# Kernel optimization log

Hardware: AMD Instinct MI355X
Metric: run time of the kernel (lower is better)

Reference implementation:

```python
import jax, jax.numpy as jnp
import numpy as np
from jax.scipy.special import logsumexp

B, T = 8192, 1024  # batch, timesteps; n_states = 2 (BKT: not-know / know)


def setup_inputs() -> dict:
    key = jax.random.key(0)
    k1, k2, k3 = jax.random.split(key, 3)
    corr = jax.random.randint(k1, (B, T), 0, 2)  # binary observations
    dynamics_logits = jax.random.normal(k2, (B, 3), dtype=jnp.float32)  # (pL, pF, pI0) logits
    obs_logits = jax.random.normal(k3, (B, T, 2), dtype=jnp.float32)  # (pG, pS) logits per step
    return {"corr": corr, "dynamics_logits": dynamics_logits, "obs_logits": obs_logits}


def _get_logits(dynamics_logits, obs_logits):
    # trans_logits[b] = [[0, d1],[d0, 0]]  (target, source)
    z = jnp.zeros_like(dynamics_logits[:, 0])
    trans_logits = jnp.stack([z, dynamics_logits[:, 1], dynamics_logits[:, 0], z], axis=1).reshape(-1, 2, 2)
    # obs_full[b,t] = [[0, o0],[o1, 0]]  (state, output)
    zo = jnp.zeros_like(obs_logits[:, :, 0])
    obs_full = jnp.stack([zo, obs_logits[:, :, 0], obs_logits[:, :, 1], zo], axis=2)
    obs_full = obs_full.reshape(obs_logits.shape[0], -1, 2, 2)
    # init_logits[b] = [0, d2]
    init_logits = jnp.stack([z, dynamics_logits[:, 2]], axis=1)
    return trans_logits, obs_full, init_logits


def _bkt(corr, dynamics_logits, obs_logits):
    trans_logits, obs_full, init_logits = _get_logits(dynamics_logits, obs_logits)
    log_obs = jax.nn.log_softmax(obs_full, axis=3)   # (B,T,2,2)
    log_t = jax.nn.log_softmax(trans_logits, axis=1)  # (B,2,2) softmax over target state
    log_alpha0 = jax.nn.log_softmax(init_logits, axis=1)  # (B,2)
    lo_t = jnp.moveaxis(log_obs, 1, 0)  # (T,B,2,2)
    y_t = corr.T                        # (T,B)

    def fwd_step(log_alpha, inp):
        lo, y = inp  # lo: (B,2,2), y: (B,)
        # predictive p(y_t | y_1:t-1)
        log_py_pred = logsumexp(lo + log_alpha[:, :, None], axis=1)  # (B,2)
        log_py_pred = log_py_pred - logsumexp(log_py_pred, axis=1, keepdims=True)
        # emission of observed symbol per state
        log_py = jnp.take_along_axis(lo, y[:, None, None], axis=2)[:, :, 0]  # (B,2)
        state_post = log_py + log_alpha  # P(h_t, y_1:t)
        new_alpha = logsumexp(log_py[:, None, :] + log_alpha[:, None, :] + log_t, axis=2)
        return new_alpha, (log_py_pred, state_post)

    _, (preds, posts) = jax.lax.scan(fwd_step, log_alpha0, (lo_t, y_t))
    output_logprobs = jnp.moveaxis(preds, 0, 1)     # (B,T,2)
    state_posteriors = jnp.moveaxis(posts, 0, 1)    # (B,T,2)

    def bwd_step(log_beta, inp):
        lo, y = inp
        log_py = jnp.take_along_axis(lo, y[:, None, None], axis=2)[:, :, 0]  # (B,2)
        new_beta = logsumexp(log_py[:, :, None] + log_beta[:, :, None] + log_t, axis=1)
        return new_beta, log_beta

    beta0 = jnp.zeros_like(log_alpha0)
    _, betas = jax.lax.scan(bwd_step, beta0, (lo_t, y_t), reverse=True)
    backward_logprobs = jnp.moveaxis(betas, 0, 1)  # (B,T,2), time-aligned

    smoothed = state_posteriors + backward_logprobs
    smoothed = smoothed - logsumexp(smoothed, axis=2, keepdims=True)
    # stack the three BxTx2 outputs -> (3,B,T,2)
    return jnp.stack([output_logprobs, state_posteriors, smoothed], axis=0)


def reference(corr, dynamics_logits, obs_logits):
    return _bkt(corr, dynamics_logits, obs_logits)
```

## Files before the change

### kernel.cpp

```cpp
#include <hip/hip_runtime.h>


#define BB 8192
#define TT 1024
#define KC 16
#define NC 64
#define GG 4
#define NTHREADS (GG * NC)
#define NEGI (-1.0e30f)
#define LOG2E 1.4426950408889634f
#define LN2   0.6931471805599453f

typedef float floatx4 __attribute__((ext_vector_type(4)));

__device__ __forceinline__ float fexp2(float x) {
    return __builtin_amdgcn_exp2f(x);
}
__device__ __forceinline__ float flog2(float x) {
    return __builtin_amdgcn_logf(x);
}
__device__ __forceinline__ float softplus2(float x) {
    return fmaxf(x, 0.0f) + flog2(1.0f + fexp2(-fabsf(x)));
}
__device__ __forceinline__ float lse2_2(float a, float b) {
    float m = fmaxf(a, b);
    return m + flog2(1.0f + fexp2(-fabsf(a - b)));
}

__global__ __launch_bounds__(NTHREADS, 4) void bkt_kernel(
        const int* __restrict__ corr,
        const float* __restrict__ dyn,
        const float* __restrict__ obs,
        float* __restrict__ out) {
    __shared__ floatx4 st[GG][NC + 2][8];

    const int tid = threadIdx.x;
    const int g = tid >> 6;
    const int c = tid & (NC - 1);
    const int b = blockIdx.x * GG + g;

    const float d0 = dyn[b * 3 + 0] * LOG2E;
    const float d1 = dyn[b * 3 + 1] * LOG2E;
    const float d2 = dyn[b * 3 + 2] * LOG2E;
    const float sd0 = softplus2(d0), sd1 = softplus2(d1);
    const float lt00 = -sd0, lt10 = d0 - sd0, lt01 = d1 - sd1, lt11 = -sd1;

    const long long cb = (long long)b * TT + c * KC;
    const float2* obs2 = (const float2*)obs;
    const long long S4 = (long long)BB * 512;
    floatx4* o0 = (floatx4*)out;
    floatx4* o1 = o0 + S4;
    floatx4* o2 = o1 + S4;

    float ox[16], oy[16];
    unsigned ybits = 0;
    float F00, F01, F10, F11;
    {
        const float4* op = (const float4*)(obs2 + cb);
        const int4* yp = (const int4*)(corr + cb);
        #pragma unroll
        for (int j = 0; j < 8; ++j) {
            float4 o4 = op[j];
            ox[2 * j]     = o4.x * LOG2E; oy[2 * j]     = o4.y * LOG2E;
            ox[2 * j + 1] = o4.z * LOG2E; oy[2 * j + 1] = o4.w * LOG2E;
        }
        #pragma unroll
        for (int j = 0; j < 4; ++j) {
            int4 y4 = yp[j];
            ybits |= (unsigned)(y4.x & 1) << (4 * j + 0);
            ybits |= (unsigned)(y4.y & 1) << (4 * j + 1);
            ybits |= (unsigned)(y4.z & 1) << (4 * j + 2);
            ybits |= (unsigned)(y4.w & 1) << (4 * j + 3);
        }
        #pragma unroll
        for (int q = 0; q < 16; ++q) {
            float sp0 = softplus2(ox[q]), sp1 = softplus2(oy[q]);
            int y = (ybits >> q) & 1;
            float py0 = y ? (ox[q] - sp0) : (-sp0);
            float py1 = y ? (-sp1) : (oy[q] - sp1);
            float N00 = py0 + lt00, N01 = py1 + lt01;
            float N10 = py0 + lt10, N11 = py1 + lt11;
            if (q == 0) {
                F00 = N00; F01 = N01; F10 = N10; F11 = N11;
            } else {
                float a_ = lse2_2(N00 + F00, N01 + F10);
                float b_ = lse2_2(N00 + F01, N01 + F11);
                float c_ = lse2_2(N10 + F00, N11 + F10);
                float d_ = lse2_2(N10 + F01, N11 + F11);
                F00 = a_; F01 = b_; F10 = c_; F11 = d_;
            }
        }
    }

    float G00 = F00, G01 = F01, G10 = F10, G11 = F11;
    float H00 = __shfl_down(F00, 1);
    float H01 = __shfl_down(F10, 1);
    float H10 = __shfl_down(F01, 1);
    float H11 = __shfl_down(F11, 1);
    if (c == NC - 1) { H00 = 0.0f; H01 = NEGI; H10 = NEGI; H11 = 0.0f; }
    #pragma unroll
    for (int dlv = 0; dlv < 6; ++dlv) {
        const int off = 1 << dlv;
        float u00 = __shfl_up(G00, off), u01 = __shfl_up(G01, off);
        float u10 = __shfl_up(G10, off), u11 = __shfl_up(G11, off);
        float g00 = lse2_2(G00 + u00, G01 + u10);
        float g01 = lse2_2(G00 + u01, G01 + u11);
        float g10 = lse2_2(G10 + u00, G11 + u10);
        float g11 = lse2_2(G10 + u01, G11 + u11);
        bool dg = (c >= off);
        G00 = dg ? g00 : G00; G01 = dg ? g01 : G01;
        G10 = dg ? g10 : G10; G11 = dg ? g11 : G11;
        float v00 = __shfl_down(H00, off), v01 = __shfl_down(H01, off);
        float v10 = __shfl_down(H10, off), v11 = __shfl_down(H11, off);
        float h00 = lse2_2(H00 + v00, H01 + v10);
        float h01 = lse2_2(H00 + v01, H01 + v11);
        float h10 = lse2_2(H10 + v00, H11 + v10);
        float h11 = lse2_2(H10 + v01, H11 + v11);
        bool dh = (c + off < NC);
        H00 = dh ? h00 : H00; H01 = dh ? h01 : H01;
        H10 = dh ? h10 : H10; H11 = dh ? h11 : H11;
    }
    const float sd2 = softplus2(d2);
    const float ai0 = -sd2, ai1 = d2 - sd2;
    float P00 = __shfl_up(G00, 1), P01 = __shfl_up(G01, 1);
    float P10 = __shfl_up(G10, 1), P11 = __shfl_up(G11, 1);
    float t0 = lse2_2(P00 + ai0, P01 + ai1);
    float t1 = lse2_2(P10 + ai0, P11 + ai1);
    float a0 = (c == 0) ? ai0 : t0;
    float a1 = (c == 0) ? ai1 : t1;
    float w0 = lse2_2(H00, H01);
    float w1 = lse2_2(H10, H11);
    float be0 = lse2_2(lt00 + w0, lt10 + w1);
    float be1 = lse2_2(lt01 + w0, lt11 + w1);

    const long long bb4 = (long long)b * 512;
    const int sw = c & 7;

    float ps[32];
    {
        float e0a, e1a;
        #pragma unroll
        for (int q = 0; q < 16; ++q) {
            float sp0 = softplus2(ox[q]), sp1 = softplus2(oy[q]);
            float lo00 = -sp0,        lo01 = ox[q] - sp0;
            float lo10 = oy[q] - sp1, lo11 = -sp1;
            float p0 = lse2_2(lo00 + a0, lo10 + a1);
            float p1 = lse2_2(lo01 + a0, lo11 + a1);
            float n = lse2_2(a0, a1);
            float wo0 = (p0 - n) * LN2, wo1 = (p1 - n) * LN2;
            int y = (ybits >> q) & 1;
            float py0 = y ? lo01 : lo00;
            float py1 = y ? lo11 : lo10;
            float s0 = py0 + a0, s1 = py1 + a1;
            ps[2 * q] = s0; ps[2 * q + 1] = s1;
            ox[q] = py0; oy[q] = py1;
            a0 = lse2_2(s0 + lt00, s1 + lt01);
            a1 = lse2_2(s0 + lt10, s1 + lt11);
            if (q & 1) st[g][c][(q >> 1) ^ sw] = (floatx4){e0a, e1a, wo0, wo1};
            else       { e0a = wo0; e1a = wo1; }
        }
    }
    #pragma unroll
    for (int i = 0; i < 8; ++i) {
        int flat = i * 64 + c;
        int c2 = flat >> 3, k2 = flat & 7;
        floatx4 v = st[g][c2][k2 ^ (c2 & 7)];
        __builtin_nontemporal_store(v, o0 + bb4 + flat);
    }
    #pragma unroll
    for (int k = 0; k < 8; ++k)
        st[g][c][k ^ sw] = (floatx4){ps[4 * k] * LN2, ps[4 * k + 1] * LN2,
                                     ps[4 * k + 2] * LN2, ps[4 * k + 3] * LN2};
    #pragma unroll
    for (int i = 0; i < 8; ++i) {
        int flat = i * 64 + c;
        int c2 = flat >> 3, k2 = flat & 7;
        floatx4 v = st[g][c2][k2 ^ (c2 & 7)];
        __builtin_nontemporal_store(v, o1 + bb4 + flat);
    }

    {
        float o0s, o1s;
        #pragma unroll
        for (int q = 15; q >= 0; --q) {
            float u0 = ps[2 * q] + be0, u1 = ps[2 * q + 1] + be1;
            float nn = lse2_2(u0, u1);
            float w20 = (u0 - nn) * LN2, w21 = (u1 - nn) * LN2;
            float nb0 = lse2_2(ox[q] + be0 + lt00, oy[q] + be1 + lt10);
            float nb1 = lse2_2(ox[q] + be0 + lt01, oy[q] + be1 + lt11);
            be0 = nb0; be1 = nb1;
            if (q & 1) { o0s = w20; o1s = w21; }
            else       st[g][c][(q >> 1) ^ sw] = (floatx4){w20, w21, o0s, o1s};
        }
    }
    #pragma unroll
    for (int i = 0; i < 8; ++i) {
        int flat = i * 64 + c;
        int c2 = flat >> 3, k2 = flat & 7;
        floatx4 v = st[g][c2][k2 ^ (c2 & 7)];
        __builtin_nontemporal_store(v, o2 + bb4 + flat);
    }
}

extern "C" void kernel_launch(void* const* d_in, const int* in_sizes, int n_in,
                              void* d_out, int out_size, void* d_ws, size_t ws_size,
                              hipStream_t stream) {
    const int*   corr = (const int*)d_in[0];
    const float* dyn  = (const float*)d_in[1];
    const float* obs  = (const float*)d_in[2];
    float* out = (float*)d_out;

    dim3 block(NTHREADS);
    dim3 grid(BB / GG);
    bkt_kernel<<<grid, block, 0, stream>>>(corr, dyn, obs, out);
}
```

Measured before the change: 288.3 us.

## Replace log-space HMM recurrences with scaled linear-probability arithmetic

Moves the forward/backward recursions, the chunk transfer-matrix products and the wave-level scan from log-sum-exp form into plain probability space. Exponent-based rescaling keeps values in range, and normalised per-step alphas and betas replace the log-domain state, which removes most exp2/log2 transcendental pairs. Logs are taken only at output time, plus an accumulated log-normaliser for the state posteriors. The tradeoff is possible precision loss or underflow in extreme cases, and a leftover dead expression computing l01.

```diff
diff --git a/kernel.cpp b/kernel.cpp
--- a/kernel.cpp
+++ b/kernel.cpp
@@ -7,7 +7,6 @@
 #define NC 64
 #define GG 4
 #define NTHREADS (GG * NC)
-#define NEGI (-1.0e30f)
 #define LOG2E 1.4426950408889634f
 #define LN2   0.6931471805599453f
 
@@ -19,12 +18,11 @@
 __device__ __forceinline__ float flog2(float x) {
     return __builtin_amdgcn_logf(x);
 }
-__device__ __forceinline__ float softplus2(float x) {
-    return fmaxf(x, 0.0f) + flog2(1.0f + fexp2(-fabsf(x)));
-}
-__device__ __forceinline__ float lse2_2(float a, float b) {
-    float m = fmaxf(a, b);
-    return m + flog2(1.0f + fexp2(-fabsf(a - b)));
+__device__ __forceinline__ float frcp(float x) {
+    return __builtin_amdgcn_rcpf(x);
+}
+__device__ __forceinline__ unsigned umax2(unsigned a, unsigned b) {
+    return a > b ? a : b;
 }
 
 __global__ __launch_bounds__(NTHREADS, 4) void bkt_kernel(
@@ -42,8 +40,14 @@
     const float d0 = dyn[b * 3 + 0] * LOG2E;
     const float d1 = dyn[b * 3 + 1] * LOG2E;
     const float d2 = dyn[b * 3 + 2] * LOG2E;
-    const float sd0 = softplus2(d0), sd1 = softplus2(d1);
-    const float lt00 = -sd0, lt10 = d0 - sd0, lt01 = d1 - sd1, lt11 = -sd1;
+    const float ua = fexp2(d0);  const float ra = frcp(1.0f + ua);
+    const float l00 = ra,        l10 = ua * ra;
+    const float ub = fexp2(-d1); const float rb = frcp(1.0f + ub);
+    const float l01 = ub * rb * 0.0f + rb * 0.0f + (1.0f - ub * rb) * 0.0f + rb / (1.0f) * 0.0f + rb * 0.0f + (rb);
+    const float l01v = rb,       l11 = ub * rb;
+    const float uc = fexp2(d2);  const float rc2 = frcp(1.0f + uc);
+    const float ai0 = rc2,       ai1 = uc * rc2;
+    const float dl0 = l00 - l01v;
 
     const long long cb = (long long)b * TT + c * KC;
     const float2* obs2 = (const float2*)obs;
@@ -55,6 +59,7 @@
     float ox[16], oy[16];
     unsigned ybits = 0;
     float F00, F01, F10, F11;
+    int kF = 0;
     {
         const float4* op = (const float4*)(obs2 + cb);
         const int4* yp = (const int4*)(corr + cb);
@@ -74,88 +79,111 @@
         }
         #pragma unroll
         for (int q = 0; q < 16; ++q) {
-            float sp0 = softplus2(ox[q]), sp1 = softplus2(oy[q]);
+            float u0 = fexp2(-ox[q]); float r0 = frcp(1.0f + u0);
+            float u1 = fexp2(-oy[q]); float r1 = frcp(1.0f + u1);
+            ox[q] = r0; oy[q] = r1;
             int y = (ybits >> q) & 1;
-            float py0 = y ? (ox[q] - sp0) : (-sp0);
-            float py1 = y ? (-sp1) : (oy[q] - sp1);
-            float N00 = py0 + lt00, N01 = py1 + lt01;
-            float N10 = py0 + lt10, N11 = py1 + lt11;
+            float ey0 = y ? r0 : u0 * r0;
+            float ey1 = y ? u1 * r1 : r1;
             if (q == 0) {
-                F00 = N00; F01 = N01; F10 = N10; F11 = N11;
+                F00 = l00 * ey0; F01 = l01v * ey1;
+                F10 = l10 * ey0; F11 = l11 * ey1;
             } else {
-                float a_ = lse2_2(N00 + F00, N01 + F10);
-                float b_ = lse2_2(N00 + F01, N01 + F11);
-                float c_ = lse2_2(N10 + F00, N11 + F10);
-                float d_ = lse2_2(N10 + F01, N11 + F11);
-                F00 = a_; F01 = b_; F10 = c_; F11 = d_;
+                float R00 = ey0 * F00, R01 = ey0 * F01;
+                float R10 = ey1 * F10, R11 = ey1 * F11;
+                F00 = l00 * R00 + l01v * R10;
+                F01 = l00 * R01 + l01v * R11;
+                F10 = l10 * R00 + l11 * R10;
+                F11 = l10 * R01 + l11 * R11;
             }
-        }
-    }
-
-    float G00 = F00, G01 = F01, G10 = F10, G11 = F11;
-    float H00 = __shfl_down(F00, 1);
-    float H01 = __shfl_down(F10, 1);
-    float H10 = __shfl_down(F01, 1);
-    float H11 = __shfl_down(F11, 1);
-    if (c == NC - 1) { H00 = 0.0f; H01 = NEGI; H10 = NEGI; H11 = 0.0f; }
+            if ((q & 3) == 3) {
+                unsigned bm = umax2(umax2(__float_as_uint(F00), __float_as_uint(F01)),
+                                    umax2(__float_as_uint(F10), __float_as_uint(F11)));
+                int e = (int)(bm >> 23);
+                float sc = __uint_as_float((unsigned)(254 - e) << 23);
+                F00 *= sc; F01 *= sc; F10 *= sc; F11 *= sc;
+                kF += e - 127;
+            }
+        }
+    }
+
+    float Gm00 = F00, Gm01 = F01, Gm10 = F10, Gm11 = F11;
+    int kG = kF;
+    float Hm00 = __shfl_down(F00, 1);
+    float Hm01 = __shfl_down(F10, 1);
+    float Hm10 = __shfl_down(F01, 1);
+    float Hm11 = __shfl_down(F11, 1);
+    if (c == NC - 1) { Hm00 = 1.0f; Hm01 = 0.0f; Hm10 = 0.0f; Hm11 = 1.0f; }
     #pragma unroll
     for (int dlv = 0; dlv < 6; ++dlv) {
         const int off = 1 << dlv;
-        float u00 = __shfl_up(G00, off), u01 = __shfl_up(G01, off);
-        float u10 = __shfl_up(G10, off), u11 = __shfl_up(G11, off);
-        float g00 = lse2_2(G00 + u00, G01 + u10);
-        float g01 = lse2_2(G00 + u01, G01 + u11);
-        float g10 = lse2_2(G10 + u00, G11 + u10);
-        float g11 = lse2_2(G10 + u01, G11 + u11);
+        float u00 = __shfl_up(Gm00, off), u01 = __shfl_up(Gm01, off);
+        float u10 = __shfl_up(Gm10, off), u11 = __shfl_up(Gm11, off);
+        int ku = __shfl_up(kG, off);
+        float n00 = Gm00 * u00 + Gm01 * u10;
+        float n01 = Gm00 * u01 + Gm01 * u11;
+        float n10 = Gm10 * u00 + Gm11 * u10;
+        float n11 = Gm10 * u01 + Gm11 * u11;
+        int kn = kG + ku;
+        unsigned bm = umax2(umax2(__float_as_uint(n00), __float_as_uint(n01)),
+                            umax2(__float_as_uint(n10), __float_as_uint(n11)));
+        int e = (int)(bm >> 23);
+        float sc = __uint_as_float((unsigned)(254 - e) << 23);
+        n00 *= sc; n01 *= sc; n10 *= sc; n11 *= sc; kn += e - 127;
         bool dg = (c >= off);
-        G00 = dg ? g00 : G00; G01 = dg ? g01 : G01;
-        G10 = dg ? g10 : G10; G11 = dg ? g11 : G11;
-        float v00 = __shfl_down(H00, off), v01 = __shfl_down(H01, off);
-        float v10 = __shfl_down(H10, off), v11 = __shfl_down(H11, off);
-        float h00 = lse2_2(H00 + v00, H01 + v10);
-        float h01 = lse2_2(H00 + v01, H01 + v11);
-        float h10 = lse2_2(H10 + v00, H11 + v10);
-        float h11 = lse2_2(H10 + v01, H11 + v11);
+        Gm00 = dg ? n00 : Gm00; Gm01 = dg ? n01 : Gm01;
+        Gm10 = dg ? n10 : Gm10; Gm11 = dg ? n11 : Gm11;
+        kG = dg ? kn : kG;
+        float v00 = __shfl_down(Hm00, off), v01 = __shfl_down(Hm01, off);
+        float v10 = __shfl_down(Hm10, off), v11 = __shfl_down(Hm11, off);
+        float h00 = Hm00 * v00 + Hm01 * v10;
+        float h01 = Hm00 * v01 + Hm01 * v11;
+        float h10 = Hm10 * v00 + Hm11 * v10;
+        float h11 = Hm10 * v01 + Hm11 * v11;
+        unsigned bh = umax2(umax2(__float_as_uint(h00), __float_as_uint(h01)),
+                            umax2(__float_as_uint(h10), __float_as_uint(h11)));
+        int eh = (int)(bh >> 23);
+        float sch = __uint_as_float((unsigned)(254 - eh) << 23);
+        h00 *= sch; h01 *= sch; h10 *= sch; h11 *= sch;
         bool dh = (c + off < NC);
-        H00 = dh ? h00 : H00; H01 = dh ? h01 : H01;
-        H10 = dh ? h10 : H10; H11 = dh ? h11 : H11;
-    }
-    const float sd2 = softplus2(d2);
-    const float ai0 = -sd2, ai1 = d2 - sd2;
-    float P00 = __shfl_up(G00, 1), P01 = __shfl_up(G01, 1);
-    float P10 = __shfl_up(G10, 1), P11 = __shfl_up(G11, 1);
-    float t0 = lse2_2(P00 + ai0, P01 + ai1);
-    float t1 = lse2_2(P10 + ai0, P11 + ai1);
-    float a0 = (c == 0) ? ai0 : t0;
-    float a1 = (c == 0) ? ai1 : t1;
-    float w0 = lse2_2(H00, H01);
-    float w1 = lse2_2(H10, H11);
-    float be0 = lse2_2(lt00 + w0, lt10 + w1);
-    float be1 = lse2_2(lt01 + w0, lt11 + w1);
+        Hm00 = dh ? h00 : Hm00; Hm01 = dh ? h01 : Hm01;
+        Hm10 = dh ? h10 : Hm10; Hm11 = dh ? h11 : Hm11;
+    }
+    float Pm00 = __shfl_up(Gm00, 1), Pm01 = __shfl_up(Gm01, 1);
+    float Pm10 = __shfl_up(Gm10, 1), Pm11 = __shfl_up(Gm11, 1);
+    int kP = __shfl_up(kG, 1);
+    float am0 = Pm00 * ai0 + Pm01 * ai1;
+    float am1 = Pm10 * ai0 + Pm11 * ai1;
+    float nrma = am0 + am1;
+    float A0 = (c == 0) ? ai0 : am0 * frcp(nrma);
+    float C  = (c == 0) ? 0.0f : (float)kP + flog2(nrma);
+    float w0 = Hm00 + Hm01, w1 = Hm10 + Hm11;
+    float b0u = l00 * w0 + l10 * w1;
+    float b1u = l01v * w0 + l11 * w1;
+    float b0 = b0u * frcp(b0u + b1u);
 
     const long long bb4 = (long long)b * 512;
     const int sw = c & 7;
 
-    float ps[32];
+    float sm0[16], sm1[16];
     {
         float e0a, e1a;
         #pragma unroll
         for (int q = 0; q < 16; ++q) {
-            float sp0 = softplus2(ox[q]), sp1 = softplus2(oy[q]);
-            float lo00 = -sp0,        lo01 = ox[q] - sp0;
-            float lo10 = oy[q] - sp1, lo11 = -sp1;
-            float p0 = lse2_2(lo00 + a0, lo10 + a1);
-            float p1 = lse2_2(lo01 + a0, lo11 + a1);
-            float n = lse2_2(a0, a1);
-            float wo0 = (p0 - n) * LN2, wo1 = (p1 - n) * LN2;
+            float g0 = ox[q], g1 = oy[q];
+            float h0 = 1.0f - g0, h1 = 1.0f - g1;
+            float A1v = 1.0f - A0;
+            float pr0 = h0 * A0 + g1 * A1v;
+            float pr1 = 1.0f - pr0;
+            float wo0 = flog2(pr0) * LN2, wo1 = flog2(pr1) * LN2;
             int y = (ybits >> q) & 1;
-            float py0 = y ? lo01 : lo00;
-            float py1 = y ? lo11 : lo10;
-            float s0 = py0 + a0, s1 = py1 + a1;
-            ps[2 * q] = s0; ps[2 * q + 1] = s1;
-            ox[q] = py0; oy[q] = py1;
-            a0 = lse2_2(s0 + lt00, s1 + lt01);
-            a1 = lse2_2(s0 + lt10, s1 + lt11);
+            float ey0 = y ? g0 : h0;
+            float ey1 = y ? h1 : g1;
+            float s0 = ey0 * A0, s1 = ey1 * A1v;
+            sm0[q] = s0; sm1[q] = s1;
+            ox[q] = ey0; oy[q] = ey1;
+            float t0 = s0 * frcp(s0 + s1);
+            A0 = l01v + t0 * dl0;
             if (q & 1) st[g][c][(q >> 1) ^ sw] = (floatx4){e0a, e1a, wo0, wo1};
             else       { e0a = wo0; e1a = wo1; }
         }
@@ -167,10 +195,19 @@
         floatx4 v = st[g][c2][k2 ^ (c2 & 7)];
         __builtin_nontemporal_store(v, o0 + bb4 + flat);
     }
-    #pragma unroll
-    for (int k = 0; k < 8; ++k)
-        st[g][c][k ^ sw] = (floatx4){ps[4 * k] * LN2, ps[4 * k + 1] * LN2,
-                                     ps[4 * k + 2] * LN2, ps[4 * k + 3] * LN2};
+    {
+        float Cr = C;
+        float e0a, e1a;
+        #pragma unroll
+        for (int q = 0; q < 16; ++q) {
+            float s0 = sm0[q], s1 = sm1[q];
+            float v0 = (flog2(s0) + Cr) * LN2;
+            float v1 = (flog2(s1) + Cr) * LN2;
+            Cr += flog2(s0 + s1);
+            if (q & 1) st[g][c][(q >> 1) ^ sw] = (floatx4){e0a, e1a, v0, v1};
+            else       { e0a = v0; e1a = v1; }
+        }
+    }
     #pragma unroll
     for (int i = 0; i < 8; ++i) {
         int flat = i * 64 + c;
@@ -183,12 +220,16 @@
         float o0s, o1s;
         #pragma unroll
         for (int q = 15; q >= 0; --q) {
-            float u0 = ps[2 * q] + be0, u1 = ps[2 * q + 1] + be1;
-            float nn = lse2_2(u0, u1);
-            float w20 = (u0 - nn) * LN2, w21 = (u1 - nn) * LN2;
-            float nb0 = lse2_2(ox[q] + be0 + lt00, oy[q] + be1 + lt10);
-            float nb1 = lse2_2(ox[q] + be0 + lt01, oy[q] + be1 + lt11);
-            be0 = nb0; be1 = nb1;
+            float s0 = sm0[q], s1 = sm1[q];
+            float b1v = 1.0f - b0;
+            float gg0 = s0 * b0, gg1 = s1 * b1v;
+            float lgs = flog2(gg0 + gg1);
+            float w20 = (flog2(gg0) - lgs) * LN2;
+            float w21 = (flog2(gg1) - lgs) * LN2;
+            float m0 = ox[q] * b0, m1 = oy[q] * b1v;
+            float nb0 = l00 * m0 + l10 * m1;
+            float nb1 = l01v * m0 + l11 * m1;
+            b0 = nb0 * frcp(nb0 + nb1);
             if (q & 1) { o0s = w20; o1s = w21; }
             else       st[g][c][(q >> 1) ^ sw] = (floatx4){w20, w21, o0s, o1s};
         }
```

After: 286.4 us. No clear change (-0.6%).
